# Optimization experiments

Measured on AMD Instinct MI355X. Metric: run time of the kernel, lower is better.

The kernel has to match this reference:

```python
import jax, jax.numpy as jnp
import numpy as np

B, L, K, D = 32, 1024, 1024, 1024

def setup_inputs() -> dict:
    key = jax.random.key(0)
    k1, k2, k3, k4, k5 = jax.random.split(key, 5)
    query = jax.random.normal(k1, (B, L, D), dtype=jnp.float32)
    context = jax.random.normal(k2, (B, K, D), dtype=jnp.float32)
    mask = jax.random.randint(k3, (B * L, K), 0, 2, dtype=jnp.int32)
    W_in = jax.random.normal(k4, (D, D), dtype=jnp.float32) * (D ** -0.5)
    W_out = jax.random.normal(k5, (D, 2 * D), dtype=jnp.float32) * ((2 * D) ** -0.5)
    return {"query": query, "context": context, "mask": mask, "W_in": W_in, "W_out": W_out}

def reference(query, context, mask, W_in, W_out):
    b, l, d = query.shape
    k = context.shape[1]
    # linear_in (general attention): q @ W_in.T
    q = jnp.einsum('bld,ed->ble', query, W_in)
    # attention scores [b, l, k]
    scores = jnp.einsum('bld,bkd->blk', q, context)
    # multiplicative-mask softmax with renormalization (masked_softmax, non-memory-efficient path)
    m = mask.astype(scores.dtype).reshape(b, l, k)
    w = jax.nn.softmax(scores * m, axis=-1) * m
    w = w / (jnp.sum(w, axis=-1, keepdims=True) + 1e-13)
    # mix attended context, concat with transformed query, project, tanh
    mix = jnp.einsum('blk,bkd->bld', w, context)
    combined = jnp.concatenate([mix, q], axis=-1)          # [b, l, 2d]
    out = jnp.tanh(jnp.einsum('blc,dc->bld', combined, W_out))
    return out
```

## Files before the change

kernel.cpp:

```cpp
#include <hip/hip_runtime.h>
#include <math.h>

typedef __bf16 bf16_t;
typedef __bf16 bf16x4 __attribute__((ext_vector_type(4)));
typedef __bf16 bf16x8 __attribute__((ext_vector_type(8)));
typedef _Float16 f16x4 __attribute__((ext_vector_type(4)));
typedef _Float16 f16x8 __attribute__((ext_vector_type(8)));
typedef float f32x4 __attribute__((ext_vector_type(4)));
typedef int i32x4 __attribute__((ext_vector_type(4)));

#define MFMA_BF16 __builtin_amdgcn_mfma_f32_16x16x32_bf16
#define MFMA_F16  __builtin_amdgcn_mfma_f32_16x16x32_f16

#define SB0 __builtin_amdgcn_sched_barrier(0)
#define LGKM(n)                                                  \
    do {                                                         \
        asm volatile("s_waitcnt lgkmcnt(" #n ")" ::: "memory");  \
        __builtin_amdgcn_sched_barrier(0);                       \
    } while (0)


__device__ __forceinline__ bf16_t to_bf16_rne(float x, float& rep) {
    unsigned u = __builtin_bit_cast(unsigned, x);
    unsigned r = u + 0x7fffu + ((u >> 16) & 1u);
    unsigned short h = (unsigned short)(r >> 16);
    rep = __builtin_bit_cast(float, ((unsigned)h) << 16);
    return __builtin_bit_cast(bf16_t, h);
}

__device__ __forceinline__ void g2l16(const void* g, void* l) {
    __builtin_amdgcn_global_load_lds(
        (const __attribute__((address_space(1))) unsigned int*)g,
        (__attribute__((address_space(3))) unsigned int*)l, 16, 0, 0);
}

__device__ __forceinline__ int lch(int r, int j) {
    return (r * 8 + (j ^ (r & 7))) * 8;
}

template <typename T>
__device__ __forceinline__ void stage2(const T* __restrict__ gA, long long ldA,
                                       const T* __restrict__ gB, long long ldB,
                                       T* buf, int tid) {
    int wid = tid >> 6, lane = tid & 63;
#pragma unroll
    for (int i = 0; i < 4; ++i) {
        int cb = i * 512 + wid * 64;
        int c = cb + lane;
        int r = c >> 3, j = (c & 7) ^ (r & 7);
        g2l16(gA + (long long)r * ldA + j * 8, buf + (size_t)cb * 8);
    }
#pragma unroll
    for (int i = 0; i < 4; ++i) {
        int cb = i * 512 + wid * 64;
        int c = cb + lane;
        int r = c >> 3, j = (c & 7) ^ (r & 7);
        g2l16(gB + (long long)r * ldB + j * 8, buf + 16384 + (size_t)cb * 8);
    }
}


__global__ __launch_bounds__(256) void split_int_k(const float* __restrict__ in,
                                                   bf16_t* __restrict__ out,
                                                   long long n4) {
    long long i = (long long)blockIdx.x * 256 + threadIdx.x;
    if (i >= n4) return;
    f32x4 v = ((const f32x4*)in)[i];
    bf16x4 hv, lv;
#pragma unroll
    for (int j = 0; j < 4; ++j) {
        float rep;
        hv[j] = to_bf16_rne(v[j], rep);
        float res = v[j] - rep;
        float rep2;
        lv[j] = to_bf16_rne(res, rep2);
    }
    long long row = i >> 8;
    int k = (int)(i & 255) * 4;
    long long base = row * 2048 + ((k >> 5) << 6) + (k & 31);
    *(bf16x4*)(out + base) = hv;
    *(bf16x4*)(out + base + 32) = lv;
}

__global__ __launch_bounds__(256) void cast_f16_k(const float* __restrict__ in,
                                                  _Float16* __restrict__ o, long long n4) {
    long long i = (long long)blockIdx.x * 256 + threadIdx.x;
    if (i >= n4) return;
    f32x4 v = ((const f32x4*)in)[i];
    f16x4 h;
#pragma unroll
    for (int j = 0; j < 4; ++j) h[j] = (_Float16)v[j];
    ((f16x4*)o)[i] = h;
}

__global__ __launch_bounds__(256) void prep_ctx_k(const float* __restrict__ ctx,
                                                  bf16_t* __restrict__ ctx_int,
                                                  _Float16* __restrict__ ctxT) {
    __shared__ _Float16 tl[32][33];
    int b = blockIdx.z;
    int k0 = blockIdx.x * 32, d0 = blockIdx.y * 32;
    const float* src = ctx + ((long long)b * 1024 + k0) * 1024 + d0;
    int x = threadIdx.x, y = threadIdx.y;
#pragma unroll
    for (int i = 0; i < 4; ++i) {
        int k = y + i * 8;
        float v = src[(long long)k * 1024 + x];
        float rep;
        bf16_t hb = to_bf16_rne(v, rep);
        float rep2;
        bf16_t lb = to_bf16_rne(v - rep, rep2);
        long long rb = ((long long)b * 1024 + k0 + k) * 2048 + d0 * 2 + x;
        ctx_int[rb] = hb;
        ctx_int[rb + 32] = lb;
        tl[x][k] = (_Float16)v;
    }
    __syncthreads();
    _Float16* dst = ctxT + ((long long)b * 1024 + d0) * 1024 + k0;
#pragma unroll
    for (int i = 0; i < 4; ++i) {
        int dd = y + i * 8;
        dst[(long long)dd * 1024 + x] = tl[dd][x];
    }
}

__global__ __launch_bounds__(256) void masked_softmax_k(const float* __restrict__ s,
                                                        const int* __restrict__ m,
                                                        _Float16* __restrict__ w) {
    long long row = blockIdx.x;
    const f32x4* sr = (const f32x4*)(s + row * 1024);
    const i32x4* mr = (const i32x4*)(m + row * 1024);
    f16x4* wr_ = (f16x4*)(w + row * 1024);
    int t = threadIdx.x;
    int lane = t & 63, wid = t >> 6;
    f32x4 v = sr[t];
    i32x4 mk = mr[t];
    float mx = -3.0e38f;
#pragma unroll
    for (int i = 0; i < 4; ++i)
        if (mk[i]) mx = fmaxf(mx, v[i]);
#pragma unroll
    for (int off = 32; off; off >>= 1) mx = fmaxf(mx, __shfl_xor(mx, off));
    __shared__ float rm[4], rs[4];
    if (!lane) rm[wid] = mx;
    __syncthreads();
    mx = fmaxf(fmaxf(rm[0], rm[1]), fmaxf(rm[2], rm[3]));
    float sum = 0.f;
    f32x4 e;
#pragma unroll
    for (int i = 0; i < 4; ++i) {
        e[i] = mk[i] ? expf(v[i] - mx) : 0.f;
        sum += e[i];
    }
#pragma unroll
    for (int off = 32; off; off >>= 1) sum += __shfl_xor(sum, off);
    if (!lane) rs[wid] = sum;
    __syncthreads();
    sum = rs[0] + rs[1] + rs[2] + rs[3];
    float inv = sum > 0.f ? 1.0f / sum : 0.f;
    f16x4 o;
#pragma unroll
    for (int i = 0; i < 4; ++i) o[i] = (_Float16)(e[i] * inv);
    wr_[t] = o;
}

template <int EPI>
__global__ __launch_bounds__(512, 2) void gemm_x3_256(
    const bf16_t* __restrict__ Aint, const bf16_t* __restrict__ Bint,
    long long sA, long long sB, long long sC, int nbx, int nby,
    float* __restrict__ Cs, bf16_t* __restrict__ Qint, _Float16* __restrict__ Qf) {
    __shared__ bf16_t lds[65536];
    const int NT = 32;
    int tid = threadIdx.x, lane = tid & 63, wid = tid >> 6;
    int wr = wid >> 2, wc = wid & 3;
    int nwg = gridDim.x;
    int bid = blockIdx.x;
    int lid = (bid & 7) * (nwg >> 3) + (bid >> 3);
    int by = lid % nby;
    int t2_ = lid / nby;
    int bx = t2_ % nbx;
    int z = t2_ / nbx;
    const bf16_t* At = Aint + (long long)z * sA + (long long)bx * 256 * 2048;
    const bf16_t* Bt = Bint + (long long)z * sB + (long long)by * 256 * 2048;
    stage2(At, 2048ll, Bt, 2048ll, lds, tid);
    stage2(At + 64, 2048ll, Bt + 64, 2048ll, lds + 32768, tid);
    f32x4 acc[8][4] = {};
    int l15 = lane & 15, l4 = lane >> 4;
    asm volatile("s_waitcnt vmcnt(8)" ::: "memory");
    SB0;
    __builtin_amdgcn_s_barrier();
    for (int t = 0; t < NT; ++t) {
        bf16_t* buf = lds + (size_t)(t & 1) * 32768;
        bf16_t* bufB = buf + 16384;
        bool st = (t + 2 < NT);
        bf16x8 bh[4], bl[4];
#pragma unroll
        for (int n = 0; n < 4; ++n) {
            int rB = wc * 64 + n * 16 + l15;
            bh[n] = *(const bf16x8*)(bufB + lch(rB, l4));
            bl[n] = *(const bf16x8*)(bufB + lch(rB, 4 + l4));
        }
        bf16x8 ah0[2], al0[2];
#pragma unroll
        for (int i = 0; i < 2; ++i) {
            int rA = wr * 128 + i * 16 + l15;
            ah0[i] = *(const bf16x8*)(buf + lch(rA, l4));
            al0[i] = *(const bf16x8*)(buf + lch(rA, 4 + l4));
        }
        SB0;
        bf16x8 ah1[2], al1[2];
#pragma unroll
        for (int i = 0; i < 2; ++i) {
            int rA = wr * 128 + (2 + i) * 16 + l15;
            ah1[i] = *(const bf16x8*)(buf + lch(rA, l4));
            al1[i] = *(const bf16x8*)(buf + lch(rA, 4 + l4));
        }
        SB0;
        LGKM(4);
        bf16x8 ah2[2], al2[2];
#pragma unroll
        for (int i = 0; i < 2; ++i) {
            int rA = wr * 128 + (4 + i) * 16 + l15;
            ah2[i] = *(const bf16x8*)(buf + lch(rA, l4));
            al2[i] = *(const bf16x8*)(buf + lch(rA, 4 + l4));
        }
        SB0;
        __builtin_amdgcn_s_setprio(1);
#pragma unroll
        for (int i = 0; i < 2; ++i)
#pragma unroll
            for (int n = 0; n < 4; ++n) {
                f32x4 a = acc[i][n];
                a = MFMA_BF16(ah0[i], bh[n], a, 0, 0, 0);
                a = MFMA_BF16(ah0[i], bl[n], a, 0, 0, 0);
                a = MFMA_BF16(al0[i], bh[n], a, 0, 0, 0);
                acc[i][n] = a;
            }
        __builtin_amdgcn_s_setprio(0);
        LGKM(4);
        bf16x8 ah3[2], al3[2];
#pragma unroll
        for (int i = 0; i < 2; ++i) {
            int rA = wr * 128 + (6 + i) * 16 + l15;
            ah3[i] = *(const bf16x8*)(buf + lch(rA, l4));
            al3[i] = *(const bf16x8*)(buf + lch(rA, 4 + l4));
        }
        SB0;
        __builtin_amdgcn_s_setprio(1);
#pragma unroll
        for (int i = 0; i < 2; ++i)
#pragma unroll
            for (int n = 0; n < 4; ++n) {
                f32x4 a = acc[2 + i][n];
                a = MFMA_BF16(ah1[i], bh[n], a, 0, 0, 0);
                a = MFMA_BF16(ah1[i], bl[n], a, 0, 0, 0);
                a = MFMA_BF16(al1[i], bh[n], a, 0, 0, 0);
                acc[2 + i][n] = a;
            }
        __builtin_amdgcn_s_setprio(0);
        LGKM(4);
        __builtin_amdgcn_s_setprio(1);
#pragma unroll
        for (int i = 0; i < 2; ++i)
#pragma unroll
            for (int n = 0; n < 4; ++n) {
                f32x4 a = acc[4 + i][n];
                a = MFMA_BF16(ah2[i], bh[n], a, 0, 0, 0);
                a = MFMA_BF16(ah2[i], bl[n], a, 0, 0, 0);
                a = MFMA_BF16(al2[i], bh[n], a, 0, 0, 0);
                acc[4 + i][n] = a;
            }
        __builtin_amdgcn_s_setprio(0);
        LGKM(0);
        __builtin_amdgcn_s_barrier();
        SB0;
        if (st)
            stage2(At + (long long)(t + 2) * 64, 2048ll,
                   Bt + (long long)(t + 2) * 64, 2048ll, buf, tid);
        __builtin_amdgcn_s_setprio(1);
#pragma unroll
        for (int i = 0; i < 2; ++i)
#pragma unroll
            for (int n = 0; n < 4; ++n) {
                f32x4 a = acc[6 + i][n];
                a = MFMA_BF16(ah3[i], bh[n], a, 0, 0, 0);
                a = MFMA_BF16(ah3[i], bl[n], a, 0, 0, 0);
                a = MFMA_BF16(al3[i], bh[n], a, 0, 0, 0);
                acc[6 + i][n] = a;
            }
        __builtin_amdgcn_s_setprio(0);
        SB0;
        if (t + 2 < NT) {
            asm volatile("s_waitcnt vmcnt(8)" ::: "memory");
        } else if (t + 1 < NT) {
            asm volatile("s_waitcnt vmcnt(0)" ::: "memory");
        }
        SB0;
        __builtin_amdgcn_s_barrier();
    }
    int r0 = bx * 256 + wr * 128 + (l4 << 2);
    int c0 = by * 256 + wc * 64 + l15;
#pragma unroll
    for (int m = 0; m < 8; ++m)
#pragma unroll
        for (int n = 0; n < 4; ++n)
#pragma unroll
            for (int j = 0; j < 4; ++j) {
                int r = r0 + m * 16 + j;
                int c = c0 + n * 16;
                float v = acc[m][n][j];
                if (EPI == 0) {
                    Cs[(long long)z * sC + (long long)r * 1024 + c] = v;
                } else {
                    float rep;
                    bf16_t hb = to_bf16_rne(v, rep);
                    float res = v - rep;
                    float rep2;
                    bf16_t lb = to_bf16_rne(res, rep2);
                    long long rb = (long long)r * 2048 + ((c >> 5) << 6) + (c & 31);
                    Qint[rb] = hb;
                    Qint[rb + 32] = lb;
                    Qf[(long long)r * 1024 + c] = (_Float16)v;
                }
            }
}

template <int EPI>
__global__ __launch_bounds__(512, 2) void gemm_f16_256(
    const _Float16* __restrict__ A1, const _Float16* __restrict__ A2,
    const _Float16* __restrict__ B,
    long long ldA, long long ldB, long long sA, long long sB, long long sC,
    int NT, int swt, int nbx, int nby,
    _Float16* __restrict__ Cm, float* __restrict__ Co) {
    __shared__ _Float16 lds[65536];
    int tid = threadIdx.x, lane = tid & 63, wid = tid >> 6;
    int wr = wid >> 2, wc = wid & 3;
    int nwg = gridDim.x;
    int bid = blockIdx.x;
    int lid = (bid & 7) * (nwg >> 3) + (bid >> 3);
    int by = lid % nby;
    int t2_ = lid / nby;
    int bx = t2_ % nbx;
    int z = t2_ / nbx;
    const _Float16* A1t = A1 + (long long)z * sA + (long long)bx * 256 * ldA;
    const _Float16* A2t = A2 + (long long)bx * 256 * ldA;
    const _Float16* Bt = B + (long long)z * sB + (long long)by * 256 * ldB;
    stage2((0 < swt) ? A1t : A2t, ldA, Bt, ldB, lds, tid);
    stage2((1 < swt) ? A1t + 64 : A2t + (long long)(1 - swt) * 64, ldA, Bt + 64, ldB,
           lds + 32768, tid);
    f32x4 acc[8][4] = {};
    int l15 = lane & 15, l4 = lane >> 4;
    asm volatile("s_waitcnt vmcnt(8)" ::: "memory");
    SB0;
    __builtin_amdgcn_s_barrier();
    for (int t = 0; t < NT; ++t) {
        _Float16* buf = lds + (size_t)(t & 1) * 32768;
        _Float16* bufB = buf + 16384;
        int tt = t + 2;
        bool st = (tt < NT);
        const _Float16* gA2 =
            (tt < swt) ? A1t + (long long)tt * 64 : A2t + (long long)(tt - swt) * 64;
        const _Float16* gB2 = Bt + (long long)tt * 64;
        f16x8 bfr[4][2];
#pragma unroll
        for (int n = 0; n < 4; ++n) {
            int rB = wc * 64 + n * 16 + l15;
#pragma unroll
            for (int ks = 0; ks < 2; ++ks)
                bfr[n][ks] = *(const f16x8*)(bufB + lch(rB, ks * 4 + l4));
        }
        f16x8 a0[2][2];
#pragma unroll
        for (int i = 0; i < 2; ++i)
#pragma unroll
            for (int ks = 0; ks < 2; ++ks) {
                int rA = wr * 128 + i * 16 + l15;
                a0[i][ks] = *(const f16x8*)(buf + lch(rA, ks * 4 + l4));
            }
        SB0;
        f16x8 a1[2][2];
#pragma unroll
        for (int i = 0; i < 2; ++i)
#pragma unroll
            for (int ks = 0; ks < 2; ++ks) {
                int rA = wr * 128 + (2 + i) * 16 + l15;
                a1[i][ks] = *(const f16x8*)(buf + lch(rA, ks * 4 + l4));
            }
        SB0;
        LGKM(4);
        f16x8 a2[2][2];
#pragma unroll
        for (int i = 0; i < 2; ++i)
#pragma unroll
            for (int ks = 0; ks < 2; ++ks) {
                int rA = wr * 128 + (4 + i) * 16 + l15;
                a2[i][ks] = *(const f16x8*)(buf + lch(rA, ks * 4 + l4));
            }
        SB0;
        __builtin_amdgcn_s_setprio(1);
#pragma unroll
        for (int i = 0; i < 2; ++i)
#pragma unroll
            for (int n = 0; n < 4; ++n) {
                f32x4 v = acc[i][n];
                v = MFMA_F16(a0[i][0], bfr[n][0], v, 0, 0, 0);
                v = MFMA_F16(a0[i][1], bfr[n][1], v, 0, 0, 0);
                acc[i][n] = v;
            }
        __builtin_amdgcn_s_setprio(0);
        LGKM(4);
        f16x8 a3[2][2];
#pragma unroll
        for (int i = 0; i < 2; ++i)
#pragma unroll
            for (int ks = 0; ks < 2; ++ks) {
                int rA = wr * 128 + (6 + i) * 16 + l15;
                a3[i][ks] = *(const f16x8*)(buf + lch(rA, ks * 4 + l4));
            }
        SB0;
        __builtin_amdgcn_s_setprio(1);
#pragma unroll
        for (int i = 0; i < 2; ++i)
#pragma unroll
            for (int n = 0; n < 4; ++n) {
                f32x4 v = acc[2 + i][n];
                v = MFMA_F16(a1[i][0], bfr[n][0], v, 0, 0, 0);
                v = MFMA_F16(a1[i][1], bfr[n][1], v, 0, 0, 0);
                acc[2 + i][n] = v;
            }
        __builtin_amdgcn_s_setprio(0);
        LGKM(4);
        __builtin_amdgcn_s_setprio(1);
#pragma unroll
        for (int i = 0; i < 2; ++i)
#pragma unroll
            for (int n = 0; n < 4; ++n) {
                f32x4 v = acc[4 + i][n];
                v = MFMA_F16(a2[i][0], bfr[n][0], v, 0, 0, 0);
                v = MFMA_F16(a2[i][1], bfr[n][1], v, 0, 0, 0);
                acc[4 + i][n] = v;
            }
        __builtin_amdgcn_s_setprio(0);
        LGKM(0);
        __builtin_amdgcn_s_barrier();
        SB0;
        if (st) stage2(gA2, ldA, gB2, ldB, buf, tid);
        __builtin_amdgcn_s_setprio(1);
#pragma unroll
        for (int i = 0; i < 2; ++i)
#pragma unroll
            for (int n = 0; n < 4; ++n) {
                f32x4 v = acc[6 + i][n];
                v = MFMA_F16(a3[i][0], bfr[n][0], v, 0, 0, 0);
                v = MFMA_F16(a3[i][1], bfr[n][1], v, 0, 0, 0);
                acc[6 + i][n] = v;
            }
        __builtin_amdgcn_s_setprio(0);
        SB0;
        if (t + 2 < NT) {
            asm volatile("s_waitcnt vmcnt(8)" ::: "memory");
        } else if (t + 1 < NT) {
            asm volatile("s_waitcnt vmcnt(0)" ::: "memory");
        }
        SB0;
        __builtin_amdgcn_s_barrier();
    }
    int r0 = bx * 256 + wr * 128 + (l4 << 2);
    int c0 = by * 256 + wc * 64 + l15;
#pragma unroll
    for (int m = 0; m < 8; ++m)
#pragma unroll
        for (int n = 0; n < 4; ++n)
#pragma unroll
            for (int j = 0; j < 4; ++j) {
                int r = r0 + m * 16 + j;
                int c = c0 + n * 16;
                float v = acc[m][n][j];
                if (EPI == 0) {
                    Cm[(long long)z * sC + (long long)r * 1024 + c] = (_Float16)v;
                } else {
                    Co[(long long)r * 1024 + c] = tanhf(v);
                }
            }
}


extern "C" void kernel_launch(void* const* d_in, const int* in_sizes, int n_in,
                              void* d_out, int out_size, void* d_ws, size_t ws_size,
                              hipStream_t stream) {
    const float* query = (const float*)d_in[0];
    const float* ctx = (const float*)d_in[1];
    const int* mask = (const int*)d_in[2];
    const float* Win = (const float*)d_in[3];
    const float* Wout = (const float*)d_in[4];
    float* outp = (float*)d_out;

    const long long MB = 1048576ll;
    int G = 1;
    if ((long long)ws_size >= 512 * MB) G = 32;
    else if ((long long)ws_size >= 256 * MB) G = 16;
    else if ((long long)ws_size >= 128 * MB) G = 8;
    else if ((long long)ws_size >= 64 * MB) G = 4;
    else if ((long long)ws_size >= 32 * MB) G = 2;

    char* p = (char*)d_ws;
    const long long R = (long long)G * 1024;
    bf16_t* qint = (bf16_t*)p; p += 4 * G * MB;
    _Float16* qf = (_Float16*)p; p += 2 * G * MB;
    char* slabA = p; p += 4 * G * MB;
    bf16_t* win_int = (bf16_t*)slabA;
    bf16_t* ctx_int = (bf16_t*)slabA;
    _Float16* wf = (_Float16*)slabA;
    _Float16* mixf = (_Float16*)(slabA + 2 * G * MB);
    _Float16* ctxT = (_Float16*)p; p += 2 * G * MB;
    char* slabC = p;
    bf16_t* qs_int = (bf16_t*)slabC;
    float* scores = (float*)slabC;
    _Float16* woutf = (_Float16*)slabC;

    const long long LD = 1048576ll;

    for (int b0 = 0; b0 < 32; b0 += G) {
        const float* qsrc = query + (long long)b0 * LD;
        const float* csrc = ctx + (long long)b0 * LD;
        split_int_k<<<1024, 256, 0, stream>>>(Win, win_int, 262144ll);
        split_int_k<<<(int)R, 256, 0, stream>>>(qsrc, qs_int, R * 256);
        gemm_x3_256<1><<<16 * G, 512, 0, stream>>>(
            qs_int, win_int, 0, 0, 0, 4 * G, 4, nullptr, qint, qf);
        prep_ctx_k<<<dim3(32, 32, G), dim3(32, 8, 1), 0, stream>>>(csrc, ctx_int, ctxT);
        gemm_x3_256<0><<<16 * G, 512, 0, stream>>>(
            qint, ctx_int, 2097152ll, 2097152ll, 1048576ll, 4, 4,
            scores, nullptr, nullptr);
        masked_softmax_k<<<(int)R, 256, 0, stream>>>(
            scores, mask + (long long)b0 * 1024 * 1024, wf);
        cast_f16_k<<<2048, 256, 0, stream>>>(Wout, woutf, 524288ll);
        gemm_f16_256<0><<<16 * G, 512, 0, stream>>>(
            wf, wf, ctxT, 1024ll, 1024ll, 1048576ll, 1048576ll, 1048576ll,
            16, 1 << 20, 4, 4, mixf, nullptr);
        gemm_f16_256<1><<<16 * G, 512, 0, stream>>>(
            mixf, qf, woutf, 1024ll, 2048ll, 0, 0, 0,
            32, 16, 4 * G, 4, nullptr, outp + (long long)b0 * LD);
    }
}
```

Measured before the change: 783.8 us.

## Double waves per GEMM block to 16 with 64x64 per-wave tiles and simpler sync

All four 256x256 GEMM kernels now launch 1024 threads instead of 512. Each wave computes a 64x64 output sub-tile instead of 128x64, so the accumulator arrays and the per-thread global-to-LDS staging loop are both halved. The fine-grained lgkmcnt-interleaved pipeline is replaced by a simpler loop: wait on vmcnt and barrier at the top, compute two sub-steps, barrier, then issue the next stage prefetch. More waves should hide latency better, but each wave loads the B fragments from LDS for less MFMA work. The launch bound of (1024,4) may also force a tight register cap and cause spills.

```diff
diff --git a/kernel.cpp b/kernel.cpp
--- a/kernel.cpp
+++ b/kernel.cpp
@@ -11,13 +11,7 @@
 
 #define MFMA_BF16 __builtin_amdgcn_mfma_f32_16x16x32_bf16
 #define MFMA_F16  __builtin_amdgcn_mfma_f32_16x16x32_f16
-
 #define SB0 __builtin_amdgcn_sched_barrier(0)
-#define LGKM(n)                                                  \
-    do {                                                         \
-        asm volatile("s_waitcnt lgkmcnt(" #n ")" ::: "memory");  \
-        __builtin_amdgcn_sched_barrier(0);                       \
-    } while (0)
 
 
 __device__ __forceinline__ bf16_t to_bf16_rne(float x, float& rep) {
@@ -44,15 +38,15 @@
                                        T* buf, int tid) {
     int wid = tid >> 6, lane = tid & 63;
 #pragma unroll
-    for (int i = 0; i < 4; ++i) {
-        int cb = i * 512 + wid * 64;
+    for (int i = 0; i < 2; ++i) {
+        int cb = i * 1024 + wid * 64;
         int c = cb + lane;
         int r = c >> 3, j = (c & 7) ^ (r & 7);
         g2l16(gA + (long long)r * ldA + j * 8, buf + (size_t)cb * 8);
     }
 #pragma unroll
-    for (int i = 0; i < 4; ++i) {
-        int cb = i * 512 + wid * 64;
+    for (int i = 0; i < 2; ++i) {
+        int cb = i * 1024 + wid * 64;
         int c = cb + lane;
         int r = c >> 3, j = (c & 7) ^ (r & 7);
         g2l16(gB + (long long)r * ldB + j * 8, buf + 16384 + (size_t)cb * 8);
@@ -164,7 +158,7 @@
 }
 
 template <int EPI>
-__global__ __launch_bounds__(512, 2) void gemm_x3_256(
+__global__ __launch_bounds__(1024, 4) void gemm_x3_256(
     const bf16_t* __restrict__ Aint, const bf16_t* __restrict__ Bint,
     long long sA, long long sB, long long sC, int nbx, int nby,
     float* __restrict__ Cs, bf16_t* __restrict__ Qint, _Float16* __restrict__ Qf) {
@@ -183,15 +177,20 @@
     const bf16_t* Bt = Bint + (long long)z * sB + (long long)by * 256 * 2048;
     stage2(At, 2048ll, Bt, 2048ll, lds, tid);
     stage2(At + 64, 2048ll, Bt + 64, 2048ll, lds + 32768, tid);
-    f32x4 acc[8][4] = {};
+    f32x4 acc[4][4] = {};
     int l15 = lane & 15, l4 = lane >> 4;
-    asm volatile("s_waitcnt vmcnt(8)" ::: "memory");
-    SB0;
-    __builtin_amdgcn_s_barrier();
     for (int t = 0; t < NT; ++t) {
         bf16_t* buf = lds + (size_t)(t & 1) * 32768;
         bf16_t* bufB = buf + 16384;
         bool st = (t + 2 < NT);
+        if (t < NT - 1) {
+            asm volatile("s_waitcnt vmcnt(4)" ::: "memory");
+        } else {
+            asm volatile("s_waitcnt vmcnt(0)" ::: "memory");
+        }
+        SB0;
+        __builtin_amdgcn_s_barrier();
+        SB0;
         bf16x8 bh[4], bl[4];
 #pragma unroll
         for (int n = 0; n < 4; ++n) {
@@ -202,28 +201,10 @@
         bf16x8 ah0[2], al0[2];
 #pragma unroll
         for (int i = 0; i < 2; ++i) {
-            int rA = wr * 128 + i * 16 + l15;
+            int rA = wr * 64 + i * 16 + l15;
             ah0[i] = *(const bf16x8*)(buf + lch(rA, l4));
             al0[i] = *(const bf16x8*)(buf + lch(rA, 4 + l4));
         }
-        SB0;
-        bf16x8 ah1[2], al1[2];
-#pragma unroll
-        for (int i = 0; i < 2; ++i) {
-            int rA = wr * 128 + (2 + i) * 16 + l15;
-            ah1[i] = *(const bf16x8*)(buf + lch(rA, l4));
-            al1[i] = *(const bf16x8*)(buf + lch(rA, 4 + l4));
-        }
-        SB0;
-        LGKM(4);
-        bf16x8 ah2[2], al2[2];
-#pragma unroll
-        for (int i = 0; i < 2; ++i) {
-            int rA = wr * 128 + (4 + i) * 16 + l15;
-            ah2[i] = *(const bf16x8*)(buf + lch(rA, l4));
-            al2[i] = *(const bf16x8*)(buf + lch(rA, 4 + l4));
-        }
-        SB0;
         __builtin_amdgcn_s_setprio(1);
 #pragma unroll
         for (int i = 0; i < 2; ++i)
@@ -236,15 +217,20 @@
                 acc[i][n] = a;
             }
         __builtin_amdgcn_s_setprio(0);
-        LGKM(4);
-        bf16x8 ah3[2], al3[2];
+        bf16x8 ah1[2], al1[2];
 #pragma unroll
         for (int i = 0; i < 2; ++i) {
-            int rA = wr * 128 + (6 + i) * 16 + l15;
-            ah3[i] = *(const bf16x8*)(buf + lch(rA, l4));
-            al3[i] = *(const bf16x8*)(buf + lch(rA, 4 + l4));
-        }
-        SB0;
+            int rA = wr * 64 + (2 + i) * 16 + l15;
+            ah1[i] = *(const bf16x8*)(buf + lch(rA, l4));
+            al1[i] = *(const bf16x8*)(buf + lch(rA, 4 + l4));
+        }
+        asm volatile("s_waitcnt lgkmcnt(0)" ::: "memory");
+        SB0;
+        __builtin_amdgcn_s_barrier();
+        SB0;
+        if (st)
+            stage2(At + (long long)(t + 2) * 64, 2048ll,
+                   Bt + (long long)(t + 2) * 64, 2048ll, buf, tid);
         __builtin_amdgcn_s_setprio(1);
 #pragma unroll
         for (int i = 0; i < 2; ++i)
@@ -257,50 +243,12 @@
                 acc[2 + i][n] = a;
             }
         __builtin_amdgcn_s_setprio(0);
-        LGKM(4);
-        __builtin_amdgcn_s_setprio(1);
-#pragma unroll
-        for (int i = 0; i < 2; ++i)
-#pragma unroll
-            for (int n = 0; n < 4; ++n) {
-                f32x4 a = acc[4 + i][n];
-                a = MFMA_BF16(ah2[i], bh[n], a, 0, 0, 0);
-                a = MFMA_BF16(ah2[i], bl[n], a, 0, 0, 0);
-                a = MFMA_BF16(al2[i], bh[n], a, 0, 0, 0);
-                acc[4 + i][n] = a;
-            }
-        __builtin_amdgcn_s_setprio(0);
-        LGKM(0);
-        __builtin_amdgcn_s_barrier();
-        SB0;
-        if (st)
-            stage2(At + (long long)(t + 2) * 64, 2048ll,
-                   Bt + (long long)(t + 2) * 64, 2048ll, buf, tid);
-        __builtin_amdgcn_s_setprio(1);
-#pragma unroll
-        for (int i = 0; i < 2; ++i)
-#pragma unroll
-            for (int n = 0; n < 4; ++n) {
-                f32x4 a = acc[6 + i][n];
-                a = MFMA_BF16(ah3[i], bh[n], a, 0, 0, 0);
-                a = MFMA_BF16(ah3[i], bl[n], a, 0, 0, 0);
-                a = MFMA_BF16(al3[i], bh[n], a, 0, 0, 0);
-                acc[6 + i][n] = a;
-            }
-        __builtin_amdgcn_s_setprio(0);
-        SB0;
-        if (t + 2 < NT) {
-            asm volatile("s_waitcnt vmcnt(8)" ::: "memory");
-        } else if (t + 1 < NT) {
-            asm volatile("s_waitcnt vmcnt(0)" ::: "memory");
-        }
-        SB0;
-        __builtin_amdgcn_s_barrier();
-    }
-    int r0 = bx * 256 + wr * 128 + (l4 << 2);
+        SB0;
+    }
+    int r0 = bx * 256 + wr * 64 + (l4 << 2);
     int c0 = by * 256 + wc * 64 + l15;
 #pragma unroll
-    for (int m = 0; m < 8; ++m)
+    for (int m = 0; m < 4; ++m)
 #pragma unroll
         for (int n = 0; n < 4; ++n)
 #pragma unroll
@@ -325,7 +273,7 @@
 }
 
 template <int EPI>
-__global__ __launch_bounds__(512, 2) void gemm_f16_256(
+__global__ __launch_bounds__(1024, 4) void gemm_f16_256(
     const _Float16* __restrict__ A1, const _Float16* __restrict__ A2,
     const _Float16* __restrict__ B,
     long long ldA, long long ldB, long long sA, long long sB, long long sC,
@@ -347,11 +295,8 @@
     stage2((0 < swt) ? A1t : A2t, ldA, Bt, ldB, lds, tid);
     stage2((1 < swt) ? A1t + 64 : A2t + (long long)(1 - swt) * 64, ldA, Bt + 64, ldB,
            lds + 32768, tid);
-    f32x4 acc[8][4] = {};
+    f32x4 acc[4][4] = {};
     int l15 = lane & 15, l4 = lane >> 4;
-    asm volatile("s_waitcnt vmcnt(8)" ::: "memory");
-    SB0;
-    __builtin_amdgcn_s_barrier();
     for (int t = 0; t < NT; ++t) {
         _Float16* buf = lds + (size_t)(t & 1) * 32768;
         _Float16* bufB = buf + 16384;
@@ -360,6 +305,14 @@
         const _Float16* gA2 =
             (tt < swt) ? A1t + (long long)tt * 64 : A2t + (long long)(tt - swt) * 64;
         const _Float16* gB2 = Bt + (long long)tt * 64;
+        if (t < NT - 1) {
+            asm volatile("s_waitcnt vmcnt(4)" ::: "memory");
+        } else {
+            asm volatile("s_waitcnt vmcnt(0)" ::: "memory");
+        }
+        SB0;
+        __builtin_amdgcn_s_barrier();
+        SB0;
         f16x8 bfr[4][2];
 #pragma unroll
         for (int n = 0; n < 4; ++n) {
@@ -373,29 +326,9 @@
         for (int i = 0; i < 2; ++i)
 #pragma unroll
             for (int ks = 0; ks < 2; ++ks) {
-                int rA = wr * 128 + i * 16 + l15;
+                int rA = wr * 64 + i * 16 + l15;
                 a0[i][ks] = *(const f16x8*)(buf + lch(rA, ks * 4 + l4));
             }
-        SB0;
-        f16x8 a1[2][2];
-#pragma unroll
-        for (int i = 0; i < 2; ++i)
-#pragma unroll
-            for (int ks = 0; ks < 2; ++ks) {
-                int rA = wr * 128 + (2 + i) * 16 + l15;
-                a1[i][ks] = *(const f16x8*)(buf + lch(rA, ks * 4 + l4));
-            }
-        SB0;
-        LGKM(4);
-        f16x8 a2[2][2];
-#pragma unroll
-        for (int i = 0; i < 2; ++i)
-#pragma unroll
-            for (int ks = 0; ks < 2; ++ks) {
-                int rA = wr * 128 + (4 + i) * 16 + l15;
-                a2[i][ks] = *(const f16x8*)(buf + lch(rA, ks * 4 + l4));
-            }
-        SB0;
         __builtin_amdgcn_s_setprio(1);
 #pragma unroll
         for (int i = 0; i < 2; ++i)
@@ -407,16 +340,19 @@
                 acc[i][n] = v;
             }
         __builtin_amdgcn_s_setprio(0);
-        LGKM(4);
-        f16x8 a3[2][2];
+        f16x8 a1[2][2];
 #pragma unroll
         for (int i = 0; i < 2; ++i)
 #pragma unroll
             for (int ks = 0; ks < 2; ++ks) {
-                int rA = wr * 128 + (6 + i) * 16 + l15;
-                a3[i][ks] = *(const f16x8*)(buf + lch(rA, ks * 4 + l4));
-            }
-        SB0;
+                int rA = wr * 64 + (2 + i) * 16 + l15;
+                a1[i][ks] = *(const f16x8*)(buf + lch(rA, ks * 4 + l4));
+            }
+        asm volatile("s_waitcnt lgkmcnt(0)" ::: "memory");
+        SB0;
+        __builtin_amdgcn_s_barrier();
+        SB0;
+        if (st) stage2(gA2, ldA, gB2, ldB, buf, tid);
         __builtin_amdgcn_s_setprio(1);
 #pragma unroll
         for (int i = 0; i < 2; ++i)
@@ -428,46 +364,12 @@
                 acc[2 + i][n] = v;
             }
         __builtin_amdgcn_s_setprio(0);
-        LGKM(4);
-        __builtin_amdgcn_s_setprio(1);
-#pragma unroll
-        for (int i = 0; i < 2; ++i)
-#pragma unroll
-            for (int n = 0; n < 4; ++n) {
-                f32x4 v = acc[4 + i][n];
-                v = MFMA_F16(a2[i][0], bfr[n][0], v, 0, 0, 0);
-                v = MFMA_F16(a2[i][1], bfr[n][1], v, 0, 0, 0);
-                acc[4 + i][n] = v;
-            }
-        __builtin_amdgcn_s_setprio(0);
-        LGKM(0);
-        __builtin_amdgcn_s_barrier();
-        SB0;
-        if (st) stage2(gA2, ldA, gB2, ldB, buf, tid);
-        __builtin_amdgcn_s_setprio(1);
-#pragma unroll
-        for (int i = 0; i < 2; ++i)
-#pragma unroll
-            for (int n = 0; n < 4; ++n) {
-                f32x4 v = acc[6 + i][n];
-                v = MFMA_F16(a3[i][0], bfr[n][0], v, 0, 0, 0);
-                v = MFMA_F16(a3[i][1], bfr[n][1], v, 0, 0, 0);
-                acc[6 + i][n] = v;
-            }
-        __builtin_amdgcn_s_setprio(0);
-        SB0;
-        if (t + 2 < NT) {
-            asm volatile("s_waitcnt vmcnt(8)" ::: "memory");
-        } else if (t + 1 < NT) {
-            asm volatile("s_waitcnt vmcnt(0)" ::: "memory");
-        }
-        SB0;
-        __builtin_amdgcn_s_barrier();
-    }
-    int r0 = bx * 256 + wr * 128 + (l4 << 2);
+        SB0;
+    }
+    int r0 = bx * 256 + wr * 64 + (l4 << 2);
     int c0 = by * 256 + wc * 64 + l15;
 #pragma unroll
-    for (int m = 0; m < 8; ++m)
+    for (int m = 0; m < 4; ++m)
 #pragma unroll
         for (int n = 0; n < 4; ++n)
 #pragma unroll
@@ -524,19 +426,19 @@
         const float* csrc = ctx + (long long)b0 * LD;
         split_int_k<<<1024, 256, 0, stream>>>(Win, win_int, 262144ll);
         split_int_k<<<(int)R, 256, 0, stream>>>(qsrc, qs_int, R * 256);
-        gemm_x3_256<1><<<16 * G, 512, 0, stream>>>(
+        gemm_x3_256<1><<<16 * G, 1024, 0, stream>>>(
             qs_int, win_int, 0, 0, 0, 4 * G, 4, nullptr, qint, qf);
         prep_ctx_k<<<dim3(32, 32, G), dim3(32, 8, 1), 0, stream>>>(csrc, ctx_int, ctxT);
-        gemm_x3_256<0><<<16 * G, 512, 0, stream>>>(
+        gemm_x3_256<0><<<16 * G, 1024, 0, stream>>>(
             qint, ctx_int, 2097152ll, 2097152ll, 1048576ll, 4, 4,
             scores, nullptr, nullptr);
         masked_softmax_k<<<(int)R, 256, 0, stream>>>(
             scores, mask + (long long)b0 * 1024 * 1024, wf);
         cast_f16_k<<<2048, 256, 0, stream>>>(Wout, woutf, 524288ll);
-        gemm_f16_256<0><<<16 * G, 512, 0, stream>>>(
+        gemm_f16_256<0><<<16 * G, 1024, 0, stream>>>(
             wf, wf, ctxT, 1024ll, 1024ll, 1048576ll, 1048576ll, 1048576ll,
             16, 1 << 20, 4, 4, mixf, nullptr);
-        gemm_f16_256<1><<<16 * G, 512, 0, stream>>>(
+        gemm_f16_256<1><<<16 * G, 1024, 0, stream>>>(
             mixf, qf, woutf, 1024ll, 2048ll, 0, 0, 0,
             32, 16, 4 * G, 4, nullptr, outp + (long long)b0 * LD);
     }
```

Result: slower. 897.3 us (+14.5%).
